# Performance work log

Measured on AMD Instinct MI355X. Metric: run time of the kernel, lower is better.

Reference implementation:

```python
import jax, jax.numpy as jnp
import numpy as np

NDIM = 3
N = 192
DX = 1.0 / N          # uniform unit box
T_REF = 300.0         # reference temperature [K]
MU_REF = 1.8e-5       # reference viscosity [Pa s]
PR = 0.72             # Prandtl number
CP = 1005.0           # specific heat [J/kg/K]


def _ddx(f, axis):
    # 2nd-order central difference, periodic BC
    return (jnp.roll(f, -1, axis) - jnp.roll(f, 1, axis)) / (2.0 * DX)


def _gradient(f):
    # scalar [N,N,N] -> [NDIM, N,N,N]
    return jnp.stack([_ddx(f, a) for a in range(NDIM)], axis=0)


def _divergence(v):
    # vector [NDIM, N,N,N] -> [N,N,N]
    out = _ddx(v[0], 0)
    for a in range(1, NDIM):
        out = out + _ddx(v[a], a)
    return out


def _viscosity(T_dim):
    return MU_REF * (T_dim / T_REF) ** 0.7


def _conductivity(T_dim):
    return _viscosity(T_dim) * CP / PR


def setup_inputs() -> dict:
    key = jax.random.key(0)
    k1, k2 = jax.random.split(key)
    u = jax.random.normal(k1, (NDIM, N, N, N), dtype=jnp.float32)
    # nondimensional temperature, kept positive for the power-law viscosity
    T = jax.random.uniform(k2, (N, N, N), dtype=jnp.float32, minval=0.5, maxval=1.5)
    return {"u": u, "T": T}


def reference(u, T):
    # --- stress tensor ---
    mu = _viscosity(T * T_REF)                                   # [N,N,N]
    # gradu[i, j] = d u_i / d x_j
    gradu = jnp.stack([_gradient(u[i]) for i in range(NDIM)], 0)  # [3,3,N,N,N]
    divu = jnp.einsum('ii...->...', gradu)                        # trace -> [N,N,N]
    S = 0.5 * (gradu + jnp.swapaxes(gradu, 0, 1))                 # symmetrized
    eye = jnp.eye(NDIM, dtype=u.dtype)[:, :, None, None, None]
    tau = 2.0 * mu * S - (2.0 / 3.0) * mu * divu * eye            # [3,3,N,N,N]

    # --- heat flux ---
    k = _conductivity(T * T_REF)
    heat_flux = -k * _gradient(T)                                 # [3,N,N,N]

    # --- assemble RHS: [mass(=0), momentum(3), energy] ---
    momentum = jnp.stack([_divergence(tau[i]) for i in range(NDIM)], 0)
    energy = -_divergence(heat_flux)
    for i in range(NDIM):
        energy = energy + _divergence(tau[i] * u[i])
    zero = jnp.zeros_like(T)
    return jnp.concatenate([zero[None], momentum, energy[None]], axis=0)
```

## Files before the change

kernel.cpp:

```cpp
#include <hip/hip_runtime.h>

#define N  192
#define N2 (N * N)
#define N3 (N * N * N)

#define TX 32
#define TY 8
#define NT 256
#define ZC 12
#define GX (N / TX)
#define GY (N / TY)
#define GZ (N / ZC)
#define NBLK (GX * GY * GZ)
#define UX (TX + 4)
#define UY (TY + 4)
#define UP (UX * UY)
#define FX (TX + 2)
#define FY (TY + 2)
#define FP (FX * FY)

static constexpr float INV2DX     = (float)N / 2.0f;
static constexpr float SCALE2     = INV2DX * INV2DX;
static constexpr float MU_REF_F   = 1.8e-5f;
static constexpr float CP_OVER_PR = 1005.0f / 0.72f;
static constexpr float TWO_THIRDS = 2.0f / 3.0f;

__device__ __forceinline__ int wrapN(int a) {
    if (a < 0)  a += N;
    if (a >= N) a -= N;
    return a;
}

struct Flux { float t00, t01, t02, t11, t12, t22, F0, F1, F2; };

__device__ __forceinline__ Flux flux_eval_reg(const float4 zm, const float4 cc,
                                              const float4 zp,
                                              const float4* __restrict__ uC, int c)
{
    const float4 xp = uC[c + 1],  xm = uC[c - 1];
    const float4 yp = uC[c + UX], ym = uC[c - UX];

    const float d00 = zp.x - zm.x;
    const float d01 = yp.x - ym.x;
    const float d02 = xp.x - xm.x;
    const float d10 = zp.y - zm.y;
    const float d11 = yp.y - ym.y;
    const float d12 = xp.y - xm.y;
    const float d20 = zp.z - zm.z;
    const float d21 = yp.z - ym.z;
    const float d22 = xp.z - xm.z;
    const float dT0 = zp.w - zm.w;
    const float dT1 = yp.w - ym.w;
    const float dT2 = xp.w - xm.w;

    const float mu   = MU_REF_F * __powf(cc.w, 0.7f);
    const float mu2  = mu + mu;
    const float divu = d00 + d11 + d22;
    const float lam  = -TWO_THIRDS * mu * divu;

    Flux f;
    f.t00 = mu2 * d00 + lam;
    f.t11 = mu2 * d11 + lam;
    f.t22 = mu2 * d22 + lam;
    f.t01 = mu * (d01 + d10);
    f.t02 = mu * (d02 + d20);
    f.t12 = mu * (d12 + d21);
    const float kc = mu * CP_OVER_PR;
    f.F0 = kc * dT0 + f.t00 * cc.x + f.t01 * cc.y + f.t02 * cc.z;
    f.F1 = kc * dT1 + f.t01 * cc.x + f.t11 * cc.y + f.t12 * cc.z;
    f.F2 = kc * dT2 + f.t02 * cc.x + f.t12 * cc.y + f.t22 * cc.z;
    return f;
}

__device__ __forceinline__ Flux flux_eval_lds(const float4* __restrict__ uM,
                                              const float4* __restrict__ uC,
                                              const float4* __restrict__ uP, int c)
{
    return flux_eval_reg(uM[c], uC[c], uP[c], uC, c);
}

__device__ __forceinline__ void sf_store(float4* __restrict__ sY, float4* __restrict__ sX,
                                         int fi, const Flux& f)
{
    sY[fi] = make_float4(f.t01, f.t11, f.t12, f.F1);
    sX[fi] = make_float4(f.t02, f.t12, f.t22, f.F2);
}

__global__ __launch_bounds__(NT)
void diffusion_zmarch_kernel(const float* __restrict__ u,
                             const float* __restrict__ Tp,
                             float* __restrict__ out)
{
    __shared__ float4 su4[3][UP];
    __shared__ float4 sfY[2][FP];
    __shared__ float4 sfX[2][FP];

    const int id  = (int)blockIdx.x;
    const int nid = (id & 7) * (NBLK / 8) + (id >> 3);
    const int bzB = nid / (GX * GY);
    const int rem = nid % (GX * GY);
    const int bx  = (rem % GX) * TX;
    const int by  = (rem / GX) * TY;
    const int z0  = bzB * ZC;

    const int tx  = threadIdx.x & (TX - 1);
    const int ty  = threadIdx.x >> 5;
    const int tid = (int)threadIdx.x;

    const float* __restrict__ u0 = u;
    const float* __restrict__ u1 = u + N3;
    const float* __restrict__ u2 = u + 2 * N3;

    const int cu = (ty + 2) * UX + (tx + 2);
    const int fi = (ty + 1) * FX + (tx + 1);

    int hfx = -1, hfy = -1;
    if (tid < TX)                 { hfy = 0;      hfx = 1 + tid; }
    else if (tid < 2 * TX)        { hfy = FY - 1; hfx = 1 + tid - TX; }
    else if (tid < 2 * TX + TY)   { hfx = 0;      hfy = 1 + tid - 2 * TX; }
    else if (tid < 2 * (TX + TY)) { hfx = FX - 1; hfy = 1 + tid - 2 * TX - TY; }
    const bool hasH = (hfx >= 0);
    const int hcu = (hfy + 1) * UX + (hfx + 1);
    const int hfi = hfy * FX + hfx;

    const int  q0   = tid;
    const int  q1   = tid + NT;
    const bool has2 = (q1 < UP);
    int ro0, ro1 = 0;
    {
        const int ux = q0 % UX, uy = q0 / UX;
        ro0 = wrapN(by + uy - 2) * N + wrapN(bx + ux - 2);
    }
    if (has2) {
        const int ux = q1 % UX, uy = q1 / UX;
        ro1 = wrapN(by + uy - 2) * N + wrapN(bx + ux - 2);
    }

#define STAGE_DIRECT(slot, zw)                                              \
    do {                                                                    \
        const int base_ = (zw) * N2;                                        \
        {  const int g_ = base_ + ro0;                                      \
           su4[slot][q0] = make_float4(u0[g_], u1[g_], u2[g_], Tp[g_]); }   \
        if (has2) {                                                         \
           const int g_ = base_ + ro1;                                      \
           su4[slot][q1] = make_float4(u0[g_], u1[g_], u2[g_], Tp[g_]); }   \
    } while (0)

    STAGE_DIRECT(0, wrapN(z0 - 2));
    STAGE_DIRECT(1, wrapN(z0 - 1));
    STAGE_DIRECT(2, z0);
    __syncthreads();

    float t00m, t01m, t02m, F0m;
    {
        const Flux fM = flux_eval_lds(su4[0], su4[1], su4[2], cu);
        t00m = fM.t00; t01m = fM.t01; t02m = fM.t02; F0m = fM.F0;
    }
    __syncthreads();
    STAGE_DIRECT(0, z0 + 1);
    __syncthreads();

    float t00c, t01c, t02c, F0c;
    {
        const Flux fC = flux_eval_lds(su4[1], su4[2], su4[0], cu);
        t00c = fC.t00; t01c = fC.t01; t02c = fC.t02; F0c = fC.F0;
        sf_store(sfY[0], sfX[0], fi, fC);
        if (hasH) {
            const Flux h = flux_eval_lds(su4[1], su4[2], su4[0], hcu);
            sf_store(sfY[0], sfX[0], hfi, h);
        }
    }
    __syncthreads();
    STAGE_DIRECT(1, z0 + 2);
    __syncthreads();

    float4 rzm = su4[2][cu];
    float4 rcc = su4[0][cu];
    float4 hzm, hcc;
    if (hasH) { hzm = su4[2][hcu]; hcc = su4[0][hcu]; }

    float4 *pC = su4[0], *pP = su4[1], *pW = su4[2];
    int cur = 1;

    int idx = z0 * N2 + (by + ty) * N + bx + tx;
    int zw  = z0 + 3; if (zw >= N) zw -= N;

    for (int it = 0; it < ZC; ++it) {
        const bool pref = (it <= ZC - 2);
        float4 r0, r1;
        if (pref) {
            const int base_ = zw * N2;
            { const int g_ = base_ + ro0;
              r0 = make_float4(u0[g_], u1[g_], u2[g_], Tp[g_]); }
            if (has2) {
              const int g_ = base_ + ro1;
              r1 = make_float4(u0[g_], u1[g_], u2[g_], Tp[g_]); }
        }

        const float4 own = pP[cu];
        const Flux fp_ = flux_eval_reg(rzm, rcc, own, pC, cu);
        float4 hown; Flux h;
        if (hasH) {
            hown = pP[hcu];
            h = flux_eval_reg(hzm, hcc, hown, pC, hcu);
        }

        const float4* __restrict__ sY = sfY[cur ^ 1];
        const float4* __restrict__ sX = sfX[cur ^ 1];
        const float4 yp = sY[fi + FX], ym = sY[fi - FX];
        const float4 xp = sX[fi + 1],  xm = sX[fi - 1];

        const float m0 = (fp_.t00 - t00m) + (yp.x - ym.x) + (xp.x - xm.x);
        const float m1 = (fp_.t01 - t01m) + (yp.y - ym.y) + (xp.y - xm.y);
        const float m2 = (fp_.t02 - t02m) + (yp.z - ym.z) + (xp.z - xm.z);
        const float en = (fp_.F0  - F0m)  + (yp.w - ym.w) + (xp.w - xm.w);

        out[idx]          = 0.0f;
        out[1 * N3 + idx] = m0 * SCALE2;
        out[2 * N3 + idx] = m1 * SCALE2;
        out[3 * N3 + idx] = m2 * SCALE2;
        out[4 * N3 + idx] = en * SCALE2;

        if (pref) { pW[q0] = r0; if (has2) pW[q1] = r1; }
        sf_store(sfY[cur], sfX[cur], fi, fp_);
        if (hasH) sf_store(sfY[cur], sfX[cur], hfi, h);

        __syncthreads();

        t00m = t00c; t01m = t01c; t02m = t02c; F0m = F0c;
        t00c = fp_.t00; t01c = fp_.t01; t02c = fp_.t02; F0c = fp_.F0;
        rzm = rcc; rcc = own;
        if (hasH) { hzm = hcc; hcc = hown; }
        float4* t = pC; pC = pP; pP = pW; pW = t;
        cur ^= 1;
        idx += N2;
        if (++zw >= N) zw = 0;
    }
#undef STAGE_DIRECT
}

extern "C" void kernel_launch(void* const* d_in, const int* in_sizes, int n_in,
                              void* d_out, int out_size, void* d_ws, size_t ws_size,
                              hipStream_t stream)
{
    const float* u   = (const float*)d_in[0];
    const float* T   = (const float*)d_in[1];
    float*       out = (float*)d_out;

    hipLaunchKernelGGL(diffusion_zmarch_kernel, dim3(NBLK), dim3(NT), 0, stream,
                       u, T, out);
}
```

Baseline: 105.2 us.

## Single-buffer flux LDS with mid-iteration barrier, nontemporal stores, memset zero plane

```diff
diff --git a/kernel.cpp b/kernel.cpp
--- a/kernel.cpp
+++ b/kernel.cpp
@@ -92,8 +92,8 @@
                              float* __restrict__ out)
 {
     __shared__ float4 su4[3][UP];
-    __shared__ float4 sfY[2][FP];
-    __shared__ float4 sfX[2][FP];
+    __shared__ float4 sfY[FP];
+    __shared__ float4 sfX[FP];
 
     const int id  = (int)blockIdx.x;
     const int nid = (id & 7) * (NBLK / 8) + (id >> 3);
@@ -164,10 +164,10 @@
     {
         const Flux fC = flux_eval_lds(su4[1], su4[2], su4[0], cu);
         t00c = fC.t00; t01c = fC.t01; t02c = fC.t02; F0c = fC.F0;
-        sf_store(sfY[0], sfX[0], fi, fC);
+        sf_store(sfY, sfX, fi, fC);
         if (hasH) {
             const Flux h = flux_eval_lds(su4[1], su4[2], su4[0], hcu);
-            sf_store(sfY[0], sfX[0], hfi, h);
+            sf_store(sfY, sfX, hfi, h);
         }
     }
     __syncthreads();
@@ -180,7 +180,6 @@
     if (hasH) { hzm = su4[2][hcu]; hcc = su4[0][hcu]; }
 
     float4 *pC = su4[0], *pP = su4[1], *pW = su4[2];
-    int cur = 1;
 
     int idx = z0 * N2 + (by + ty) * N + bx + tx;
     int zw  = z0 + 3; if (zw >= N) zw -= N;
@@ -197,33 +196,31 @@
               r1 = make_float4(u0[g_], u1[g_], u2[g_], Tp[g_]); }
         }
 
+        const float4 yp = sfY[fi + FX], ym = sfY[fi - FX];
+        const float4 xp = sfX[fi + 1],  xm = sfX[fi - 1];
         const float4 own = pP[cu];
+        float4 hown;
+        if (hasH) hown = pP[hcu];
+
+        asm volatile("s_waitcnt lgkmcnt(0)\n\ts_barrier" ::: "memory");
+
         const Flux fp_ = flux_eval_reg(rzm, rcc, own, pC, cu);
-        float4 hown; Flux h;
-        if (hasH) {
-            hown = pP[hcu];
-            h = flux_eval_reg(hzm, hcc, hown, pC, hcu);
-        }
-
-        const float4* __restrict__ sY = sfY[cur ^ 1];
-        const float4* __restrict__ sX = sfX[cur ^ 1];
-        const float4 yp = sY[fi + FX], ym = sY[fi - FX];
-        const float4 xp = sX[fi + 1],  xm = sX[fi - 1];
+        Flux h;
+        if (hasH) h = flux_eval_reg(hzm, hcc, hown, pC, hcu);
 
         const float m0 = (fp_.t00 - t00m) + (yp.x - ym.x) + (xp.x - xm.x);
         const float m1 = (fp_.t01 - t01m) + (yp.y - ym.y) + (xp.y - xm.y);
         const float m2 = (fp_.t02 - t02m) + (yp.z - ym.z) + (xp.z - xm.z);
         const float en = (fp_.F0  - F0m)  + (yp.w - ym.w) + (xp.w - xm.w);
 
-        out[idx]          = 0.0f;
-        out[1 * N3 + idx] = m0 * SCALE2;
-        out[2 * N3 + idx] = m1 * SCALE2;
-        out[3 * N3 + idx] = m2 * SCALE2;
-        out[4 * N3 + idx] = en * SCALE2;
-
+        __builtin_nontemporal_store(m0 * SCALE2, &out[1 * N3 + idx]);
+        __builtin_nontemporal_store(m1 * SCALE2, &out[2 * N3 + idx]);
+        __builtin_nontemporal_store(m2 * SCALE2, &out[3 * N3 + idx]);
+        __builtin_nontemporal_store(en * SCALE2, &out[4 * N3 + idx]);
+
+        sf_store(sfY, sfX, fi, fp_);
+        if (hasH) sf_store(sfY, sfX, hfi, h);
         if (pref) { pW[q0] = r0; if (has2) pW[q1] = r1; }
-        sf_store(sfY[cur], sfX[cur], fi, fp_);
-        if (hasH) sf_store(sfY[cur], sfX[cur], hfi, h);
 
         __syncthreads();
 
@@ -232,7 +229,6 @@
         rzm = rcc; rcc = own;
         if (hasH) { hzm = hcc; hcc = hown; }
         float4* t = pC; pC = pP; pP = pW; pW = t;
-        cur ^= 1;
         idx += N2;
         if (++zw >= N) zw = 0;
     }
@@ -247,6 +243,8 @@
     const float* T   = (const float*)d_in[1];
     float*       out = (float*)d_out;
 
+    hipMemsetAsync(out, 0, (size_t)N3 * sizeof(float), stream);
+
     hipLaunchKernelGGL(diffusion_zmarch_kernel, dim3(NBLK), dim3(NT), 0, stream,
                        u, T, out);
 }
```

Measured after the change: 101.8 us. -3.2%, faster.
